# Kernel optimization log

Measured on AMD Instinct MI355X. Metric: run time of the kernel, lower is better.

Reference implementation:

```python
import jax, jax.numpy as jnp
import numpy as np


def conv2d(x, w, groups=1, pad=0):
    # x: [N,C,H,W], w: [O, C//groups, kh, kw]
    return jax.lax.conv_general_dilated(
        x, w, window_strides=(1, 1), padding=[(pad, pad), (pad, pad)],
        dimension_numbers=("NCHW", "OIHW", "NCHW"), feature_group_count=groups)


def l2norm(x, eps=1e-12):
    # torch F.normalize over last dim: x / max(||x||_2, eps)
    n = jnp.sqrt(jnp.sum(x * x, axis=-1, keepdims=True))
    return x / jnp.maximum(n, eps)


def setup_inputs() -> dict:
    key = jax.random.key(0)
    dim, heads, b, H, W = 48, 8, 2, 256, 256
    ks = jax.random.split(key, 20)
    rn = lambda k, shp, s: (jax.random.normal(k, shp, dtype=jnp.float32) * s)
    return {
        "x1": rn(ks[0], (b, dim, H, W), 1.0),
        "x2": rn(ks[1], (b, dim, H, W), 1.0),
        "t1": jnp.ones((heads, 1, 1), jnp.float32),
        "t2": jnp.ones((heads, 1, 1), jnp.float32),
        "qkv1_w": rn(ks[2], (dim * 3, dim, 1, 1), 0.05),
        "qkv1_dw": rn(ks[3], (dim * 3, 1, 3, 3), 0.05),
        "qkv2_w": rn(ks[4], (dim * 3, dim, 1, 1), 0.05),
        "qkv2_dw": rn(ks[5], (dim * 3, 1, 3, 3), 0.05),
        "mid1_w": rn(ks[6], (dim, dim, 1, 1), 0.05),
        "mid2_w": rn(ks[7], (dim, dim, 1, 1), 0.05),
        "pE_w": rn(ks[8], (dim * 8, dim * 2, 1, 1), 0.05),
        "pE_dw": rn(ks[9], (dim * 8, 1, 3, 3), 0.05),
        "pE1_w": rn(ks[10], (dim * 4, dim, 1, 1), 0.05),
        "pE1_dw": rn(ks[11], (dim * 4, 1, 3, 3), 0.05),
        "pE2_w": rn(ks[12], (dim * 4, dim, 1, 1), 0.05),
        "pE2_dw": rn(ks[13], (dim * 4, 1, 3, 3), 0.05),
        "po1_w": rn(ks[14], (dim * 2, dim * 4, 1, 1), 0.05),
        "po2_w": rn(ks[15], (dim * 2, dim * 4, 1, 1), 0.05),
    }


def reference(x1, x2, t1, t2, qkv1_w, qkv1_dw, qkv2_w, qkv2_dw,
              mid1_w, mid2_w, pE_w, pE_dw, pE1_w, pE1_dw,
              pE2_w, pE2_dw, po1_w, po2_w):
    b, c, h, w = x1.shape
    heads = t1.shape[0]
    ch = c // heads  # channels per head

    def to_heads(t):  # [b, c, h, w] -> [b, heads, ch, h*w]
        return t.reshape(b, heads, ch, h * w)

    qkv1 = conv2d(conv2d(x1, qkv1_w), qkv1_dw, groups=3 * c, pad=1)
    q1, k1, v1 = jnp.split(qkv1, 3, axis=1)
    qkv2 = conv2d(conv2d(x2, qkv2_w), qkv2_dw, groups=3 * c, pad=1)
    q2, k2, v2 = jnp.split(qkv2, 3, axis=1)

    q1, k1, v1 = to_heads(q1), to_heads(k1), to_heads(v1)
    q2, k2, v2 = to_heads(q2), to_heads(k2), to_heads(v2)
    q1, k1 = l2norm(q1), l2norm(k1)
    q2, k2 = l2norm(q2), l2norm(k2)

    # channel cross-attention: [b, heads, ch, ch]
    attn1 = jnp.einsum("bhcn,bhdn->bhcd", q2, k1) * t1
    attn2 = jnp.einsum("bhcn,bhdn->bhcd", q1, k2) * t2
    out1 = jnp.einsum("bhcd,bhdn->bhcn", jax.nn.softmax(attn1, axis=-1), v1)
    out2 = jnp.einsum("bhcd,bhdn->bhcn", jax.nn.softmax(attn2, axis=-1), v2)
    out1 = out1.reshape(b, c, h, w)
    out2 = out2.reshape(b, c, h, w)

    x1 = x1 + conv2d(out1, mid1_w)
    x2 = x2 + conv2d(out2, mid2_w)
    out = jnp.concatenate([x1, x2], axis=1)  # [b, 2c, h, w]

    g = conv2d(conv2d(out, pE_w), pE_dw, groups=8 * c, pad=1)  # [b, 8c, h, w]
    g1, g2 = jnp.split(g, 2, axis=1)
    x1 = jax.nn.gelu(g1, approximate=False) * conv2d(conv2d(x1, pE1_w), pE1_dw, groups=4 * c, pad=1)
    x2 = jax.nn.gelu(g2, approximate=False) * conv2d(conv2d(x2, pE2_w), pE2_dw, groups=4 * c, pad=1)

    return out + conv2d(x1, po1_w) + conv2d(x2, po2_w)
```

## Files before the change

kernel.cpp:

```cpp
#include <hip/hip_runtime.h>
#include <math.h>

#define HW_ 65536

typedef __attribute__((ext_vector_type(8))) short b16x8;
typedef __attribute__((ext_vector_type(4))) short b16x4;
typedef __attribute__((ext_vector_type(4))) float f32x4;

__device__ __forceinline__ unsigned short f2b(float f) {
    union { float f; unsigned u; } v; v.f = f;
    unsigned r = v.u + 0x7fffu + ((v.u >> 16) & 1u);
    return (unsigned short)(r >> 16);
}
__device__ __forceinline__ float b2f(unsigned short h) {
    union { unsigned u; float f; } v; v.u = ((unsigned)h) << 16; return v.f;
}
__device__ __forceinline__ float gelu_f(float x) {
    float t = 0.7978845608f * fmaf(0.044715f * x, x * x, x);
    float e = __expf(2.f * t);
    float th = 1.f - 2.f / (e + 1.f);
    return 0.5f * x * (1.f + th);
}

__device__ __forceinline__ float wave_reduce_sum(float v) {
    #pragma unroll
    for (int off = 32; off; off >>= 1) v += __shfl_down(v, off, 64);
    return v;
}

__device__ __forceinline__ size_t baddr(long px, int CC, int g) {
    return (((size_t)(px >> 4)) * CC + g) * 128 + ((size_t)(px & 15) << 3);
}

__global__ __launch_bounds__(256) void wprep_k(
    const float* __restrict__ q1w, const float* __restrict__ q2w,
    const float* __restrict__ m1w, const float* __restrict__ m2w,
    const float* __restrict__ pEw, const float* __restrict__ p1w,
    const float* __restrict__ p2w, const float* __restrict__ o1w,
    const float* __restrict__ o2w,
    const float* __restrict__ q1dw, const float* __restrict__ q2dw,
    const float* __restrict__ pEdw, const float* __restrict__ p1dw,
    const float* __restrict__ p2dw,
    unsigned short* __restrict__ wt, float* __restrict__ dwt)
{
    const int idx = blockIdx.x * 256 + threadIdx.x;
    if (idx < 135168) {
        const int base[8] = {0,9216,18432,21504,24576,61440,98304,116736};
        int s = 0;
        #pragma unroll
        for (int i = 1; i < 8; i++) if (idx >= base[i]) s = i;
        const int local = idx - base[s];
        float v = 0.f;
        if (s < 4) {
            const int m = local >> 6, k = local & 63;
            const float* src = (s == 0) ? q1w : (s == 1) ? q2w : (s == 2) ? m1w : m2w;
            if (k < 48) v = src[m * 48 + k];
        } else if (s < 6) {
            const int br = s - 4;
            const int m = local / 96, k = local % 96;
            if (m < 192) {
                v = pEw[(size_t)(br * 192 + m) * 96 + k];
            } else {
                const float* p12 = br ? p2w : p1w;
                const int lo = br * 48, m2 = m - 192;
                if (k >= lo && k < lo + 48) v = p12[m2 * 48 + (k - lo)];
            }
        } else {
            const int m = local / 192, k = local % 192;
            v = ((s == 6) ? o1w : o2w)[m * 192 + k];
        }
        wt[idx] = f2b(v);
    } else if (idx < 135168 + 9504) {
        const int d = idx - 135168;
        const int dbase[5] = {0,1296,2592,6048,7776};
        const int Cs[5] = {144,144,384,192,192};
        int s = 0;
        #pragma unroll
        for (int i = 1; i < 5; i++) if (d >= dbase[i]) s = i;
        const int local = d - dbase[s], C = Cs[s];
        const int t = local / C, c = local % C;
        const float* src = (s == 0) ? q1dw : (s == 1) ? q2dw : (s == 2) ? pEdw
                         : (s == 3) ? p1dw : p2dw;
        dwt[d] = src[c * 9 + t];
    }
}

template<int BM, int KC, int NT, int BSRC, int EPI, bool GRIDSWAP>
__global__ __launch_bounds__(256) void gemm_k(
    const unsigned short* __restrict__ B16,
    const float* __restrict__ Bf32, int Cin,
    const unsigned short* __restrict__ W16,
    unsigned short* __restrict__ out16, int CCo, int Coff,
    float* __restrict__ outf, const unsigned short* __restrict__ res)
{
    constexpr int MF = BM / 16;
    const int tid = threadIdx.x;
    const int lane = tid & 63, w = tid >> 6;
    const int lm = lane & 15, lk = lane >> 4;
    const int mb = GRIDSWAP ? blockIdx.x : blockIdx.y;
    const int pxblk = GRIDSWAP ? blockIdx.y : blockIdx.x;
    const int m0 = mb * BM;
    const long wavepx = ((long)pxblk * 4 + w) * (NT * 16);
    const long pxb0 = wavepx >> 4;

    f32x4 acc[NT][MF];
    #pragma unroll
    for (int nt = 0; nt < NT; nt++)
        #pragma unroll
        for (int m = 0; m < MF; m++)
            #pragma unroll
            for (int j = 0; j < 4; j++) acc[nt][m][j] = 0.f;

    #pragma unroll
    for (int kc = 0; kc < KC; kc++) {
        b16x8 a[MF];
        #pragma unroll
        for (int m = 0; m < MF; m++)
            a[m] = *(const b16x8*)&W16[(size_t)(m0 + m * 16 + lm) * (KC * 32) + kc * 32 + lk * 8];
        #pragma unroll
        for (int nt = 0; nt < NT; nt++) {
            b16x8 bb;
            if (BSRC == 0) {
                bb = *(const b16x8*)&B16[((pxb0 + nt) * (KC * 4) + (kc * 4 + lk)) * 128 + lm * 8];
            } else {
                const long px = wavepx + nt * 16 + lm;
                const int p = (int)(px & 65535), bat = (int)(px >> 16);
                #pragma unroll
                for (int j = 0; j < 8; j++) {
                    const int c = kc * 32 + lk * 8 + j;
                    float v = (c < Cin) ? Bf32[((size_t)(bat * Cin + c) << 16) + p] : 0.f;
                    bb[j] = (short)f2b(v);
                }
            }
            #pragma unroll
            for (int m = 0; m < MF; m++)
                acc[nt][m] = __builtin_amdgcn_mfma_f32_16x16x32_bf16(a[m], bb, acc[nt][m], 0, 0, 0);
        }
    }

    #pragma unroll
    for (int nt = 0; nt < NT; nt++) {
        const long px = wavepx + nt * 16 + lm;
        #pragma unroll
        for (int m = 0; m < MF; m++) {
            const int mrow = m * 16 + lk * 4;
            if (EPI == 0) {
                b16x4 o;
                #pragma unroll
                for (int j = 0; j < 4; j++) o[j] = (short)f2b(acc[nt][m][j]);
                const int ch = Coff + m0 + mrow;
                *(b16x4*)&out16[((pxb0 + nt) * CCo + (ch >> 3)) * 128 + lm * 8 + (ch & 7)] = o;
            } else if (EPI == 1) {
                const int p = (int)(px & 65535), bat = (int)(px >> 16);
                b16x4 r4 = *(const b16x4*)&res[((pxb0 + nt) * 12 + (mrow >> 3)) * 128 + lm * 8 + (mrow & 7)];
                #pragma unroll
                for (int j = 0; j < 4; j++)
                    outf[((size_t)(bat * 96 + mrow + j) << 16) + p]
                        = acc[nt][m][j] + b2f((unsigned short)r4[j]);
            } else {
                const int p = (int)(px & 65535), bat = (int)(px >> 16);
                #pragma unroll
                for (int j = 0; j < 4; j++) {
                    const size_t adr = ((size_t)(bat * 96 + mrow + j) << 16) + p;
                    outf[adr] += acc[nt][m][j];
                }
            }
        }
    }
}

__device__ __forceinline__ void dw_acc8(
    float acc[4][8], const unsigned short* __restrict__ T, int CC, int g,
    long px0, int y, int x0, const float* __restrict__ wt, int wstr)
{
    #pragma unroll
    for (int dy = -1; dy <= 1; dy++) {
        const int yy = y + dy;
        if ((unsigned)yy >= 256u) continue;
        float w[3][8];
        #pragma unroll
        for (int t = 0; t < 3; t++) {
            const float* wp = wt + (size_t)((dy + 1) * 3 + t) * wstr;
            const float4 a = *(const float4*)wp;
            const float4 b = *(const float4*)(wp + 4);
            w[t][0] = a.x; w[t][1] = a.y; w[t][2] = a.z; w[t][3] = a.w;
            w[t][4] = b.x; w[t][5] = b.y; w[t][6] = b.z; w[t][7] = b.w;
        }
        #pragma unroll
        for (int c = 0; c < 6; c++) {
            const int xx = x0 - 1 + c;
            b16x8 v;
            if ((unsigned)xx < 256u) {
                v = *(const b16x8*)&T[baddr(px0 + dy * 256 + (c - 1), CC, g)];
            } else {
                #pragma unroll
                for (int k = 0; k < 8; k++) v[k] = 0;
            }
            float f[8];
            #pragma unroll
            for (int k = 0; k < 8; k++) f[k] = b2f((unsigned short)v[k]);
            const int ilo = (c - 2 < 0) ? 0 : c - 2;
            const int ihi = (c < 3) ? c : 3;
            #pragma unroll
            for (int i = ilo; i <= ihi; i++)
                #pragma unroll
                for (int j = 0; j < 8; j++)
                    acc[i][j] = fmaf(w[c - i][j], f[j], acc[i][j]);
        }
    }
}

__global__ __launch_bounds__(256) void dw144_k(
    const unsigned short* __restrict__ in1, unsigned short* __restrict__ out1,
    const unsigned short* __restrict__ in2, unsigned short* __restrict__ out2,
    const float* __restrict__ dwt)
{
    const int z = blockIdx.z;
    const unsigned short* in = z ? in2 : in1;
    unsigned short* out = z ? out2 : out1;
    const float* wt = dwt + z * 1296;
    const int bx = blockIdx.x;
    const int sb = (bx & 7) * 288 + (bx >> 3);
    const int idx = sb * 256 + threadIdx.x;
    const int pb = idx / 72;
    const int rem = idx - pb * 72;
    const int g = rem >> 2, i = rem & 3;
    const long px0 = (long)pb * 16 + i * 4;
    const int y = (int)((px0 & 65535) >> 8), x0 = (int)(px0 & 255);

    float acc[4][8];
    #pragma unroll
    for (int a = 0; a < 4; a++)
        #pragma unroll
        for (int j = 0; j < 8; j++) acc[a][j] = 0.f;
    dw_acc8(acc, in, 18, g, px0, y, x0, wt + g * 8, 144);
    #pragma unroll
    for (int a = 0; a < 4; a++) {
        b16x8 o;
        #pragma unroll
        for (int j = 0; j < 8; j++) o[j] = (short)f2b(acc[a][j]);
        *(b16x8*)&out[baddr(px0 + a, 18, g)] = o;
    }
}

__global__ __launch_bounds__(256) void dwtail_k(
    const unsigned short* __restrict__ GH, unsigned short* __restrict__ Xg,
    const float* __restrict__ dwtG, const float* __restrict__ dwtH)
{
    const int bx = blockIdx.x;
    const int sb = (bx & 7) * 384 + (bx >> 3);
    const int idx = sb * 256 + threadIdx.x;
    const int pb = idx / 96;
    const int rem = idx - pb * 96;
    const int g = rem >> 2, i = rem & 3;
    const long px0 = (long)pb * 16 + i * 4;
    const int y = (int)((px0 & 65535) >> 8), x0 = (int)(px0 & 255);

    float aG[4][8], aH[4][8];
    #pragma unroll
    for (int a = 0; a < 4; a++)
        #pragma unroll
        for (int j = 0; j < 8; j++) { aG[a][j] = 0.f; aH[a][j] = 0.f; }
    dw_acc8(aG, GH, 48, g,      px0, y, x0, dwtG + g * 8, 384);
    dw_acc8(aH, GH, 48, 24 + g, px0, y, x0, dwtH + g * 8, 192);

    #pragma unroll
    for (int a = 0; a < 4; a++) {
        b16x8 o;
        #pragma unroll
        for (int j = 0; j < 8; j++)
            o[j] = (short)f2b(gelu_f(aG[a][j]) * aH[a][j]);
        *(b16x8*)&Xg[baddr(px0 + a, 24, g)] = o;
    }
}

__global__ __launch_bounds__(256) void attnA_k(
    const unsigned short* __restrict__ Q1, const unsigned short* __restrict__ Q2,
    float* __restrict__ part)
{
    const int tid = threadIdx.x;
    const int chunk = blockIdx.x, bh = blockIdx.y, a = blockIdx.z;
    const int b = bh >> 3, h = bh & 7;
    const unsigned* Qq = (const unsigned*)(a ? Q1 : Q2);
    const unsigned* Qk = (const unsigned*)(a ? Q2 : Q1);
    const int u0 = h * 3;
    const int cq = u0 >> 2, o = u0 & 3;
    const int ck = (24 + u0) >> 2;

    float dot[36], nq[6], nk[6];
    #pragma unroll
    for (int i = 0; i < 36; i++) dot[i] = 0.f;
    #pragma unroll
    for (int i = 0; i < 6; i++) { nq[i] = 0.f; nk[i] = 0.f; }

    #pragma unroll 1
    for (int r = 0; r < 8; r++) {
        const long px = (long)b * 65536 + chunk * 2048 + r * 256 + tid;
        const size_t rowu = ((size_t)(px >> 4)) * 18 * 64 + ((px & 15) << 2);
        const uint4 qa = *(const uint4*)&Qq[rowu + (size_t)cq * 64];
        const uint4 qb = *(const uint4*)&Qq[rowu + (size_t)(cq + 1) * 64];
        const uint4 ka = *(const uint4*)&Qk[rowu + (size_t)ck * 64];
        const uint4 kb = *(const uint4*)&Qk[rowu + (size_t)(ck + 1) * 64];
        unsigned uq[3], uk[3];
        if (o == 0)      { uq[0]=qa.x; uq[1]=qa.y; uq[2]=qa.z; uk[0]=ka.x; uk[1]=ka.y; uk[2]=ka.z; }
        else if (o == 1) { uq[0]=qa.y; uq[1]=qa.z; uq[2]=qa.w; uk[0]=ka.y; uk[1]=ka.z; uk[2]=ka.w; }
        else if (o == 2) { uq[0]=qa.z; uq[1]=qa.w; uq[2]=qb.x; uk[0]=ka.z; uk[1]=ka.w; uk[2]=kb.x; }
        else             { uq[0]=qa.w; uq[1]=qb.x; uq[2]=qb.y; uk[0]=ka.w; uk[1]=kb.x; uk[2]=kb.y; }
        float q[6], k[6];
        #pragma unroll
        for (int i = 0; i < 3; i++) {
            union { unsigned u; float f; } lo, hi;
            lo.u = uq[i] << 16; hi.u = uq[i] & 0xFFFF0000u;
            q[2 * i] = lo.f; q[2 * i + 1] = hi.f;
            lo.u = uk[i] << 16; hi.u = uk[i] & 0xFFFF0000u;
            k[2 * i] = lo.f; k[2 * i + 1] = hi.f;
        }
        #pragma unroll
        for (int c = 0; c < 6; c++) nq[c] = fmaf(q[c], q[c], nq[c]);
        #pragma unroll
        for (int d = 0; d < 6; d++) nk[d] = fmaf(k[d], k[d], nk[d]);
        #pragma unroll
        for (int c = 0; c < 6; c++)
            #pragma unroll
            for (int d = 0; d < 6; d++) dot[c * 6 + d] = fmaf(q[c], k[d], dot[c * 6 + d]);
    }

    __shared__ float red[4][48];
    const int lane = tid & 63, wid = tid >> 6;
    #pragma unroll
    for (int i = 0; i < 48; i++) {
        float v = (i < 36) ? dot[i] : (i < 42 ? nq[i - 36] : nk[i - 42]);
        v = wave_reduce_sum(v);
        if (!lane) red[wid][i] = v;
    }
    __syncthreads();
    if (tid < 48)
        part[((size_t)((a * 16 + bh) * 32 + chunk)) * 48 + tid]
            = red[0][tid] + red[1][tid] + red[2][tid] + red[3][tid];
}

__global__ void attnB_k(const float* __restrict__ part,
                        const float* __restrict__ t1, const float* __restrict__ t2,
                        float* __restrict__ att)
{
    const int abh = blockIdx.x, tid = threadIdx.x;
    const int a = abh >> 4, b = (abh >> 3) & 1, h = abh & 7;
    __shared__ float s[48];
    if (tid < 48) {
        float v = 0.f;
        for (int ch = 0; ch < 32; ch++) v += part[((size_t)abh * 32 + ch) * 48 + tid];
        s[tid] = v;
    }
    __syncthreads();
    if (tid < 6) {
        const int c = tid;
        const float tv = a ? t2[h] : t1[h];
        const float qn = fmaxf(sqrtf(s[36 + c]), 1e-12f);
        float raw[6];
        #pragma unroll
        for (int d = 0; d < 6; d++)
            raw[d] = tv * s[c * 6 + d] / (qn * fmaxf(sqrtf(s[42 + d]), 1e-12f));
        float m = raw[0];
        #pragma unroll
        for (int d = 1; d < 6; d++) m = fmaxf(m, raw[d]);
        float e[6], sum = 0.f;
        #pragma unroll
        for (int d = 0; d < 6; d++) { e[d] = expf(raw[d] - m); sum += e[d]; }
        const float inv = 1.f / sum;
        #pragma unroll
        for (int d = 0; d < 6; d++)
            att[((size_t)(a * 2 + b) * 8 + h) * 36 + c * 6 + d] = e[d] * inv;
    }
}

__global__ __launch_bounds__(256) void mid_k(
    const unsigned short* __restrict__ Q1, const unsigned short* __restrict__ Q2,
    const float* __restrict__ att,
    const float* __restrict__ x1, const float* __restrict__ x2,
    const unsigned short* __restrict__ Wm, unsigned short* __restrict__ D16p)
{
    const int br = blockIdx.y;
    const unsigned short* Qv = br ? Q2 : Q1;
    const float* x = br ? x2 : x1;
    const unsigned short* W16 = Wm + br * 3072;
    const float* attb = att + br * 576;
    const int boff = br * 48;

    __shared__ float atts[288];
    __shared__ unsigned short S[256][72];
    const int tid = threadIdx.x;
    const long px = (long)blockIdx.x * 256 + tid;
    const int bat = (int)(px >> 16);

    for (int i = tid; i < 288; i += 256) atts[i] = attb[bat * 288 + i];

    float v[48];
    #pragma unroll
    for (int i = 0; i < 6; i++) {
        b16x8 t = *(const b16x8*)&Qv[baddr(px, 18, 12 + i)];
        #pragma unroll
        for (int j = 0; j < 8; j++) v[i * 8 + j] = b2f((unsigned short)t[j]);
    }
    __syncthreads();

    #pragma unroll
    for (int h = 0; h < 8; h++) {
        unsigned short sh[6];
        #pragma unroll
        for (int c = 0; c < 6; c++) {
            float s = 0.f;
            #pragma unroll
            for (int d = 0; d < 6; d++) s = fmaf(atts[h * 36 + c * 6 + d], v[h * 6 + d], s);
            sh[c] = f2b(s);
        }
        #pragma unroll
        for (int i = 0; i < 3; i++) {
            unsigned packed = (unsigned)sh[2 * i] | ((unsigned)sh[2 * i + 1] << 16);
            *(unsigned*)&S[tid][h * 6 + 2 * i] = packed;
        }
    }
    #pragma unroll
    for (int i = 0; i < 8; i++) *(unsigned*)&S[tid][48 + 2 * i] = 0u;
    __syncthreads();

    const int lane = tid & 63, w = tid >> 6;
    const int lm = lane & 15, lk = lane >> 4;
    f32x4 acc[4][3];
    #pragma unroll
    for (int nt = 0; nt < 4; nt++)
        #pragma unroll
        for (int m = 0; m < 3; m++)
            #pragma unroll
            for (int j = 0; j < 4; j++) acc[nt][m][j] = 0.f;

    #pragma unroll
    for (int kc = 0; kc < 2; kc++) {
        b16x8 a[3];
        #pragma unroll
        for (int m = 0; m < 3; m++)
            a[m] = *(const b16x8*)&W16[(size_t)(m * 16 + lm) * 64 + kc * 32 + lk * 8];
        #pragma unroll
        for (int nt = 0; nt < 4; nt++) {
            b16x8 bb = *(const b16x8*)&S[w * 64 + nt * 16 + lm][kc * 32 + lk * 8];
            #pragma unroll
            for (int m = 0; m < 3; m++)
                acc[nt][m] = __builtin_amdgcn_mfma_f32_16x16x32_bf16(a[m], bb, acc[nt][m], 0, 0, 0);
        }
    }

    #pragma unroll
    for (int nt = 0; nt < 4; nt++) {
        const long px2 = (long)blockIdx.x * 256 + w * 64 + nt * 16 + lm;
        const int p2 = (int)(px2 & 65535);
        const long pxb2 = px2 >> 4;
        #pragma unroll
        for (int m = 0; m < 3; m++) {
            const int row = m * 16 + lk * 4;
            b16x4 o;
            #pragma unroll
            for (int j = 0; j < 4; j++) {
                float xv = x[((size_t)(bat * 48 + row + j) << 16) + p2];
                o[j] = (short)f2b(acc[nt][m][j] + xv);
            }
            const int ch = boff + row;
            *(b16x4*)&D16p[(pxb2 * 12 + (ch >> 3)) * 128 + lm * 8 + (ch & 7)] = o;
        }
    }
}

extern "C" void kernel_launch(void* const* d_in, const int* in_sizes, int n_in,
                              void* d_out, int out_size, void* d_ws, size_t ws_size,
                              hipStream_t stream) {
    const float* x1      = (const float*)d_in[0];
    const float* x2      = (const float*)d_in[1];
    const float* t1      = (const float*)d_in[2];
    const float* t2      = (const float*)d_in[3];
    const float* qkv1_w  = (const float*)d_in[4];
    const float* qkv1_dw = (const float*)d_in[5];
    const float* qkv2_w  = (const float*)d_in[6];
    const float* qkv2_dw = (const float*)d_in[7];
    const float* mid1_w  = (const float*)d_in[8];
    const float* mid2_w  = (const float*)d_in[9];
    const float* pE_w    = (const float*)d_in[10];
    const float* pE_dw   = (const float*)d_in[11];
    const float* pE1_w   = (const float*)d_in[12];
    const float* pE1_dw  = (const float*)d_in[13];
    const float* pE2_w   = (const float*)d_in[14];
    const float* pE2_dw  = (const float*)d_in[15];
    const float* po1_w   = (const float*)d_in[16];
    const float* po2_w   = (const float*)d_in[17];
    float* dout = (float*)d_out;
    char* ws = (char*)d_ws;

    unsigned short* D16p  = (unsigned short*)(ws + 0);
    unsigned short* QKVc1 = (unsigned short*)(ws + 25165824);
    unsigned short* QKVc2 = (unsigned short*)(ws + 62914560);
    unsigned short* Q1    = (unsigned short*)(ws + 100663296);
    unsigned short* Q2    = (unsigned short*)(ws + 138412032);
    unsigned short* GH    = (unsigned short*)(ws + 25165824);
    unsigned short* Xg    = (unsigned short*)(ws + 125829120);
    float*          PART  = (float*)(ws + 176160768);
    float*          ATT   = (float*)(ws + 176357376);
    unsigned short* W16   = (unsigned short*)(ws + 176361984);
    float*          DWT   = (float*)(ws + 176632320);

    const dim3 blk(256);

    wprep_k<<<dim3(566), blk, 0, stream>>>(
        qkv1_w, qkv2_w, mid1_w, mid2_w, pE_w, pE1_w, pE2_w, po1_w, po2_w,
        qkv1_dw, qkv2_dw, pE_dw, pE1_dw, pE2_dw, W16, DWT);

    gemm_k<144,2,4,1,0,false><<<dim3(512,1), blk, 0, stream>>>(
        nullptr, x1, 48, W16, QKVc1, 18, 0, nullptr, nullptr);
    gemm_k<144,2,4,1,0,false><<<dim3(512,1), blk, 0, stream>>>(
        nullptr, x2, 48, W16 + 9216, QKVc2, 18, 0, nullptr, nullptr);
    dw144_k<<<dim3(2304,1,2), blk, 0, stream>>>(QKVc1, Q1, QKVc2, Q2, DWT);

    attnA_k<<<dim3(32,16,2), blk, 0, stream>>>(Q1, Q2, PART);
    attnB_k<<<dim3(32), dim3(64), 0, stream>>>(PART, t1, t2, ATT);

    mid_k<<<dim3(512,2), blk, 0, stream>>>(Q1, Q2, ATT, x1, x2, W16 + 18432, D16p);

    for (int br = 0; br < 2; br++) {
        gemm_k<192,3,2,0,0,true><<<dim3(2,1024), blk, 0, stream>>>(
            D16p, nullptr, 0, W16 + 24576 + br * 36864, GH, 48, 0,
            nullptr, nullptr);
        dwtail_k<<<dim3(3072), blk, 0, stream>>>(
            GH, Xg, DWT + 2592 + br * 192, DWT + (br ? 7776 : 6048));
        if (br == 0)
            gemm_k<96,6,4,0,1,false><<<dim3(512,1), blk, 0, stream>>>(
                Xg, nullptr, 0, W16 + 98304, nullptr, 0, 0, dout, D16p);
        else
            gemm_k<96,6,4,0,2,false><<<dim3(512,1), blk, 0, stream>>>(
                Xg, nullptr, 0, W16 + 116736, nullptr, 0, 0, dout, nullptr);
    }
}
```

Baseline: 411.9 us.

## Rewrite depthwise tail to 8-pixel sliding rows and retune GEMM tiling

Result: slower. 463.0 us (+12.4%).

```diff
diff --git a/kernel.cpp b/kernel.cpp
--- a/kernel.cpp
+++ b/kernel.cpp
@@ -243,34 +243,95 @@
     }
 }
 
+__device__ __forceinline__ void dw_row8(
+    float acc[8][8], const unsigned short* __restrict__ T,
+    size_t cb, size_t lb, size_t rb, bool lval, bool rval,
+    const float* __restrict__ wt, int wstr, int tapbase)
+{
+    float w[3][8];
+    #pragma unroll
+    for (int tx = 0; tx < 3; tx++) {
+        const float* wp = wt + (size_t)(tapbase + tx) * wstr;
+        const float4 a = *(const float4*)wp;
+        const float4 b = *(const float4*)(wp + 4);
+        w[tx][0] = a.x; w[tx][1] = a.y; w[tx][2] = a.z; w[tx][3] = a.w;
+        w[tx][4] = b.x; w[tx][5] = b.y; w[tx][6] = b.z; w[tx][7] = b.w;
+    }
+    #pragma unroll
+    for (int c = 0; c < 10; c++) {
+        b16x8 v;
+        const bool valid = (c == 0) ? lval : (c == 9) ? rval : true;
+        const size_t addr = (c == 0) ? lb : (c == 9) ? rb : (cb + (size_t)(c - 1) * 8);
+        if (valid) v = *(const b16x8*)&T[addr];
+        else {
+            #pragma unroll
+            for (int k = 0; k < 8; k++) v[k] = 0;
+        }
+        float f[8];
+        #pragma unroll
+        for (int k = 0; k < 8; k++) f[k] = b2f((unsigned short)v[k]);
+        #pragma unroll
+        for (int tx = 0; tx < 3; tx++) {
+            const int p = c - tx;
+            if (p >= 0 && p < 8)
+                #pragma unroll
+                for (int j = 0; j < 8; j++)
+                    acc[p][j] = fmaf(w[tx][j], f[j], acc[p][j]);
+        }
+    }
+}
+
 __global__ __launch_bounds__(256) void dwtail_k(
     const unsigned short* __restrict__ GH, unsigned short* __restrict__ Xg,
     const float* __restrict__ dwtG, const float* __restrict__ dwtH)
 {
     const int bx = blockIdx.x;
-    const int sb = (bx & 7) * 384 + (bx >> 3);
-    const int idx = sb * 256 + threadIdx.x;
-    const int pb = idx / 96;
-    const int rem = idx - pb * 96;
-    const int g = rem >> 2, i = rem & 3;
-    const long px0 = (long)pb * 16 + i * 4;
-    const int y = (int)((px0 & 65535) >> 8), x0 = (int)(px0 & 255);
-
-    float aG[4][8], aH[4][8];
-    #pragma unroll
-    for (int a = 0; a < 4; a++)
-        #pragma unroll
-        for (int j = 0; j < 8; j++) { aG[a][j] = 0.f; aH[a][j] = 0.f; }
-    dw_acc8(aG, GH, 48, g,      px0, y, x0, dwtG + g * 8, 384);
-    dw_acc8(aH, GH, 48, 24 + g, px0, y, x0, dwtH + g * 8, 192);
-
-    #pragma unroll
-    for (int a = 0; a < 4; a++) {
+    const int sb = (bx & 7) * 192 + (bx >> 3);
+    const int t = sb * 256 + threadIdx.x;
+    const int g = t % 24;
+    const int r = t / 24;
+    const long px0 = (long)r * 8;
+    const int y = (int)((px0 >> 8) & 255);
+    const int x0 = (int)(px0 & 255);
+    const bool lval = (x0 > 0), rval = (x0 < 248);
+
+    float aG[8][8], aH[8][8];
+    #pragma unroll
+    for (int p = 0; p < 8; p++)
+        #pragma unroll
+        for (int j = 0; j < 8; j++) { aG[p][j] = 0.f; aH[p][j] = 0.f; }
+
+    #pragma unroll
+    for (int dy = -1; dy <= 1; dy++) {
+        const int yy = y + dy;
+        if ((unsigned)yy >= 256u) continue;
+        const long pc = px0 + (long)dy * 256;
+        const long pb = pc >> 4;
+        const int half = (int)((pc >> 3) & 1);
+        const int tapb = (dy + 1) * 3;
+        {
+            const size_t cb = ((size_t)pb * 48 + g) * 128 + (size_t)half * 64;
+            const size_t lb = half ? cb - 8 : ((size_t)(pb - 1) * 48 + g) * 128 + 120;
+            const size_t rb = half ? ((size_t)(pb + 1) * 48 + g) * 128 : cb + 64;
+            dw_row8(aG, GH, cb, lb, rb, lval, rval, dwtG + g * 8, 384, tapb);
+        }
+        {
+            const int gg = 24 + g;
+            const size_t cb = ((size_t)pb * 48 + gg) * 128 + (size_t)half * 64;
+            const size_t lb = half ? cb - 8 : ((size_t)(pb - 1) * 48 + gg) * 128 + 120;
+            const size_t rb = half ? ((size_t)(pb + 1) * 48 + gg) * 128 : cb + 64;
+            dw_row8(aH, GH, cb, lb, rb, lval, rval, dwtH + g * 8, 192, tapb);
+        }
+    }
+
+    const size_t ob = (((size_t)(px0 >> 4)) * 24 + g) * 128 + (size_t)((px0 >> 3) & 1) * 64;
+    #pragma unroll
+    for (int p = 0; p < 8; p++) {
         b16x8 o;
         #pragma unroll
         for (int j = 0; j < 8; j++)
-            o[j] = (short)f2b(gelu_f(aG[a][j]) * aH[a][j]);
-        *(b16x8*)&Xg[baddr(px0 + a, 24, g)] = o;
+            o[j] = (short)f2b(gelu_f(aG[p][j]) * aH[p][j]);
+        *(b16x8*)&Xg[ob + (size_t)p * 8] = o;
     }
 }
 
@@ -510,9 +571,9 @@
         qkv1_w, qkv2_w, mid1_w, mid2_w, pE_w, pE1_w, pE2_w, po1_w, po2_w,
         qkv1_dw, qkv2_dw, pE_dw, pE1_dw, pE2_dw, W16, DWT);
 
-    gemm_k<144,2,4,1,0,false><<<dim3(512,1), blk, 0, stream>>>(
+    gemm_k<144,2,2,1,0,false><<<dim3(1024,1), blk, 0, stream>>>(
         nullptr, x1, 48, W16, QKVc1, 18, 0, nullptr, nullptr);
-    gemm_k<144,2,4,1,0,false><<<dim3(512,1), blk, 0, stream>>>(
+    gemm_k<144,2,2,1,0,false><<<dim3(1024,1), blk, 0, stream>>>(
         nullptr, x2, 48, W16 + 9216, QKVc2, 18, 0, nullptr, nullptr);
     dw144_k<<<dim3(2304,1,2), blk, 0, stream>>>(QKVc1, Q1, QKVc2, Q2, DWT);
 
@@ -522,16 +583,16 @@
     mid_k<<<dim3(512,2), blk, 0, stream>>>(Q1, Q2, ATT, x1, x2, W16 + 18432, D16p);
 
     for (int br = 0; br < 2; br++) {
-        gemm_k<192,3,2,0,0,true><<<dim3(2,1024), blk, 0, stream>>>(
+        gemm_k<96,3,2,0,0,true><<<dim3(4,1024), blk, 0, stream>>>(
             D16p, nullptr, 0, W16 + 24576 + br * 36864, GH, 48, 0,
             nullptr, nullptr);
-        dwtail_k<<<dim3(3072), blk, 0, stream>>>(
+        dwtail_k<<<dim3(1536), blk, 0, stream>>>(
             GH, Xg, DWT + 2592 + br * 192, DWT + (br ? 7776 : 6048));
         if (br == 0)
-            gemm_k<96,6,4,0,1,false><<<dim3(512,1), blk, 0, stream>>>(
+            gemm_k<96,6,2,0,1,false><<<dim3(1024,1), blk, 0, stream>>>(
                 Xg, nullptr, 0, W16 + 98304, nullptr, 0, 0, dout, D16p);
         else
-            gemm_k<96,6,4,0,2,false><<<dim3(512,1), blk, 0, stream>>>(
+            gemm_k<96,6,2,0,2,false><<<dim3(1024,1), blk, 0, stream>>>(
                 Xg, nullptr, 0, W16 + 116736, nullptr, 0, 0, dout, nullptr);
     }
 }
```
